# Performance work log

Hardware: AMD Instinct MI355X
Metric: run time of the kernel (lower is better)

## Reference

```python
import jax, jax.numpy as jnp
import numpy as np

N = 100000
E = 3200000
F_IN = 256
D_OUT = 128


def setup_inputs() -> dict:
    key = jax.random.key(0)
    ks = jax.random.split(key, 12)
    x = jax.random.normal(ks[0], (N, F_IN), dtype=jnp.float32)
    adj_val = jax.random.uniform(ks[1], (E,), dtype=jnp.float32)
    edge_row = jnp.sort(jax.random.randint(ks[2], (E,), 0, N))
    edge_col = jax.random.randint(ks[3], (E,), 0, N)
    # learned params (glorot-ish scaling)
    W1 = jax.random.normal(ks[4], (F_IN, D_OUT), dtype=jnp.float32) * (1.0 / np.sqrt(F_IN))   # conv1d_1 (1x1, no bias)
    w2 = jax.random.normal(ks[5], (D_OUT, 1), dtype=jnp.float32) * (1.0 / np.sqrt(D_OUT))     # conv1d_2
    b2 = jnp.zeros((1,), dtype=jnp.float32)
    w3 = jax.random.normal(ks[6], (D_OUT, 1), dtype=jnp.float32) * (1.0 / np.sqrt(D_OUT))     # conv1d_3
    b3 = jnp.zeros((1,), dtype=jnp.float32)
    kernel = jax.random.normal(ks[7], (F_IN, D_OUT), dtype=jnp.float32) * (1.0 / np.sqrt(F_IN))
    bias = jax.random.normal(ks[8], (N, D_OUT), dtype=jnp.float32) * 0.02
    return {"x": x, "adj_val": adj_val, "W1": W1, "w2": w2, "b2": b2,
            "w3": w3, "b3": b3, "kernel": kernel, "bias": bias,
            "edge_row": edge_row, "edge_col": edge_col}


def reference(x, adj_val, W1, w2, b2, w3, b3, kernel, bias, edge_row, edge_col):
    # 1x1 conv projections (equivalent to per-node dense layers)
    mapped = x @ W1                                   # [N, D]
    sa1 = (mapped @ w2 + b2)[:, 0]                    # [N]
    sa2 = (mapped @ w3 + b3)[:, 0]                    # [N]
    # sparse*dense broadcast then sparse add: per edge (i,j):
    #   adj_val * sa1[i] + adj_val * sa2[j]
    e = adj_val * (sa1[edge_row] + sa2[edge_col])     # [E]
    e = jax.nn.leaky_relu(e, negative_slope=0.2)
    # sparse row-wise softmax over nonzero entries
    m = jax.ops.segment_max(e, edge_row, num_segments=N)        # [N]
    m = jnp.where(jnp.isfinite(m), m, 0.0)
    ex = jnp.exp(e - m[edge_row])                               # [E]
    denom = jax.ops.segment_sum(ex, edge_row, num_segments=N)   # [N]
    denom = jnp.where(denom > 0, denom, 1.0)
    att = ex / denom[edge_row]                                  # [E]
    # dense feature transform then SpMM aggregation
    value = x @ kernel                                          # [N, D_OUT]
    out = jax.ops.segment_sum(att[:, None] * value[edge_col], edge_row, num_segments=N)
    out = out + bias                                            # use_bias=True
    return out  # activation=None (linear), single head, 'average' reduction
```

## Files before the change

### kernel.cpp

```cpp
#include <hip/hip_runtime.h>
#include <math.h>

#define N_NODES 100000
#define N_EDGES 3200000
#define F_IN    256
#define D_OUT   128

typedef __attribute__((ext_vector_type(8))) short short8;
typedef __attribute__((ext_vector_type(4))) float f32x4;

__device__ __forceinline__ unsigned short f2bf(float f) {
    unsigned u = __float_as_uint(f);
    unsigned r = (u + 0x7FFFu + ((u >> 16) & 1u)) >> 16;
    return (unsigned short)r;
}

__device__ __forceinline__ float dot4(f32x4 a, f32x4 b) {
    return a.x * b.x + a.y * b.y + a.z * b.z + a.w * b.w;
}

__device__ __forceinline__ float sb(unsigned u, int k) {
    return (float)((int)(u << ((3 - k) * 8)) >> 24);
}

__global__ __launch_bounds__(128) void prep_kernel(
    const float* __restrict__ W1, const float* __restrict__ w2,
    const float* __restrict__ w3, const float* __restrict__ kern,
    float* __restrict__ v1, float* __restrict__ v2,
    unsigned short* __restrict__ kbT) {
    const int kk  = blockIdx.x;
    const int tid = threadIdx.x;
    kbT[(size_t)tid * F_IN + kk] = f2bf(kern[(size_t)kk * D_OUT + tid]);
    if (tid < 64) {
        const float* wr = W1 + (size_t)kk * D_OUT;
        float a = wr[tid], b = wr[tid + 64];
        float s1 = a * w2[tid] + b * w2[tid + 64];
        float s2 = a * w3[tid] + b * w3[tid + 64];
#pragma unroll
        for (int o = 32; o > 0; o >>= 1) {
            s1 += __shfl_xor(s1, o);
            s2 += __shfl_xor(s2, o);
        }
        if (tid == 0) { v1[kk] = s1; v2[kk] = s2; }
    }
}

__global__ void row_ptr_kernel(const int* __restrict__ edge_row,
                               int* __restrict__ row_ptr) {
    int r = blockIdx.x * blockDim.x + threadIdx.x;
    if (r > N_NODES) return;
    int lo = 0, hi = N_EDGES;
    while (lo < hi) {
        int mid = (lo + hi) >> 1;
        if (edge_row[mid] < r) lo = mid + 1; else hi = mid;
    }
    row_ptr[r] = lo;
}

__global__ __launch_bounds__(256) void gemm_sa_kernel(
    const float* __restrict__ x, const unsigned short* __restrict__ kbT,
    const float* __restrict__ v1, const float* __restrict__ v2,
    const float* __restrict__ b2p, const float* __restrict__ b3p,
    signed char* __restrict__ valq, float* __restrict__ scale,
    float* __restrict__ sa1, float* __restrict__ sa2) {
    const int wid = blockIdx.x * 4 + (threadIdx.x >> 6);
    const int m_base = wid * 32;
    if (m_base >= N_NODES) return;
    const int lane = threadIdx.x & 63;
    const int r = lane & 15;
    const int q = lane >> 4;

    const f32x4* x0 = (const f32x4*)(x + (size_t)(m_base + r) * F_IN + q * 8);
    const f32x4* x1 = (const f32x4*)(x + (size_t)(m_base + 16 + r) * F_IN + q * 8);

    f32x4 acc[2][8];
#pragma unroll
    for (int t = 0; t < 2; ++t)
#pragma unroll
        for (int nt = 0; nt < 8; ++nt) acc[t][nt] = (f32x4)(0.f);
    float s1a = 0.f, s1b = 0.f, s2a = 0.f, s2b = 0.f;

#pragma unroll 2
    for (int s = 0; s < 8; ++s) {
        f32x4 p00 = __builtin_nontemporal_load(x0 + s * 8);
        f32x4 p01 = __builtin_nontemporal_load(x0 + s * 8 + 1);
        f32x4 p10 = __builtin_nontemporal_load(x1 + s * 8);
        f32x4 p11 = __builtin_nontemporal_load(x1 + s * 8 + 1);
        const f32x4* vp1 = (const f32x4*)(v1 + s * 32 + q * 8);
        const f32x4* vp2 = (const f32x4*)(v2 + s * 32 + q * 8);
        f32x4 va = vp1[0], vb = vp1[1], vc = vp2[0], vd = vp2[1];
        s1a += dot4(p00, va) + dot4(p01, vb);
        s2a += dot4(p00, vc) + dot4(p01, vd);
        s1b += dot4(p10, va) + dot4(p11, vb);
        s2b += dot4(p10, vc) + dot4(p11, vd);

        short8 a0, a1;
        a0[0] = (short)f2bf(p00.x); a0[1] = (short)f2bf(p00.y);
        a0[2] = (short)f2bf(p00.z); a0[3] = (short)f2bf(p00.w);
        a0[4] = (short)f2bf(p01.x); a0[5] = (short)f2bf(p01.y);
        a0[6] = (short)f2bf(p01.z); a0[7] = (short)f2bf(p01.w);
        a1[0] = (short)f2bf(p10.x); a1[1] = (short)f2bf(p10.y);
        a1[2] = (short)f2bf(p10.z); a1[3] = (short)f2bf(p10.w);
        a1[4] = (short)f2bf(p11.x); a1[5] = (short)f2bf(p11.y);
        a1[6] = (short)f2bf(p11.z); a1[7] = (short)f2bf(p11.w);

#pragma unroll
        for (int nt = 0; nt < 8; ++nt) {
            const short8 b = *(const short8*)(kbT + (size_t)(nt * 16 + r) * F_IN
                                              + s * 32 + q * 8);
            acc[0][nt] = __builtin_amdgcn_mfma_f32_16x16x32_bf16(a0, b, acc[0][nt], 0, 0, 0);
            acc[1][nt] = __builtin_amdgcn_mfma_f32_16x16x32_bf16(a1, b, acc[1][nt], 0, 0, 0);
        }
    }

    s1a += __shfl_xor(s1a, 16); s1a += __shfl_xor(s1a, 32);
    s1b += __shfl_xor(s1b, 16); s1b += __shfl_xor(s1b, 32);
    s2a += __shfl_xor(s2a, 16); s2a += __shfl_xor(s2a, 32);
    s2b += __shfl_xor(s2b, 16); s2b += __shfl_xor(s2b, 32);
    if (q == 0) {
        float bb2 = b2p[0], bb3 = b3p[0];
        sa1[m_base + r]      = s1a + bb2;
        sa1[m_base + 16 + r] = s1b + bb2;
        sa2[m_base + r]      = s2a + bb3;
        sa2[m_base + 16 + r] = s2b + bb3;
    }

#pragma unroll
    for (int t = 0; t < 2; ++t)
#pragma unroll
        for (int reg = 0; reg < 4; ++reg) {
            float m = 0.f;
#pragma unroll
            for (int nt = 0; nt < 8; ++nt) m = fmaxf(m, fabsf(acc[t][nt][reg]));
            m = fmaxf(m, __shfl_xor(m, 1));
            m = fmaxf(m, __shfl_xor(m, 2));
            m = fmaxf(m, __shfl_xor(m, 4));
            m = fmaxf(m, __shfl_xor(m, 8));
            const int row = m_base + t * 16 + q * 4 + reg;
            const float inv = m > 0.f ? 127.f / m : 0.f;
            if (r == 0) scale[row] = m * (1.f / 127.f);
#pragma unroll
            for (int nt = 0; nt < 8; ++nt) {
                int iq = (int)rintf(acc[t][nt][reg] * inv);
                valq[(size_t)row * D_OUT + nt * 16 + r] = (signed char)iq;
            }
        }
}

__global__ __launch_bounds__(256) void attn_agg_kernel(
    const int* __restrict__ row_ptr, const int* __restrict__ edge_col,
    const float* __restrict__ adj, const float* __restrict__ sa1,
    const float* __restrict__ sa2, const signed char* __restrict__ valq,
    const float* __restrict__ scale, const float* __restrict__ bias,
    float* __restrict__ out) {
    const int lane = threadIdx.x & 63;
    int row = blockIdx.x * 4 + (threadIdx.x >> 6);
    if (row >= N_NODES) return;
    row = __builtin_amdgcn_readfirstlane(row);

    const int s   = row_ptr[row];
    const int cnt = row_ptr[row + 1] - s;
    const float sa1r = sa1[row];

    const int g = lane >> 4;
    const int r = lane & 15;
    const signed char* vbase = valq + r * 8;

    float acc[8];
#pragma unroll
    for (int j = 0; j < 8; ++j) acc[j] = 0.f;
    float sum = 0.f;

    for (int base = 0; base < cnt; base += 64) {
        const int n = min(64, cnt - base);

        int c = 0;
        float w = 0.f;
        if (lane < n) {
            const int e = s + base + lane;
            c = __builtin_nontemporal_load(edge_col + e);
            const float a = __builtin_nontemporal_load(adj + e);
            float t = a * (sa1r + sa2[c]);
            t = fmaxf(t, 0.2f * t);
            const float ex = __expf(t);
            sum += ex;
            w = ex * scale[c];
        }

#pragma unroll 4
        for (int i = 0; i < n; i += 4) {
            const int   cc = __shfl(c, i + g);
            const float ww = __shfl(w, i + g);
            const uint2 p = *(const uint2*)(vbase + (size_t)cc * D_OUT);
            acc[0] += ww * sb(p.x, 0); acc[1] += ww * sb(p.x, 1);
            acc[2] += ww * sb(p.x, 2); acc[3] += ww * sb(p.x, 3);
            acc[4] += ww * sb(p.y, 0); acc[5] += ww * sb(p.y, 1);
            acc[6] += ww * sb(p.y, 2); acc[7] += ww * sb(p.y, 3);
        }
    }

    sum += __shfl_xor(sum, 1);
    sum += __shfl_xor(sum, 2);
    sum += __shfl_xor(sum, 4);
    sum += __shfl_xor(sum, 8);
#pragma unroll
    for (int o = 16; o < 64; o <<= 1) {
        sum += __shfl_xor(sum, o);
#pragma unroll
        for (int j = 0; j < 8; ++j) acc[j] += __shfl_xor(acc[j], o);
    }
    const float inv = sum > 0.f ? 1.f / sum : 1.f;

    if (g == 0) {
        const f32x4* bp = (const f32x4*)(bias + (size_t)row * D_OUT + r * 8);
        f32x4 b0 = __builtin_nontemporal_load(bp);
        f32x4 b1 = __builtin_nontemporal_load(bp + 1);
        f32x4 r0, r1;
        r0.x = acc[0] * inv + b0.x; r0.y = acc[1] * inv + b0.y;
        r0.z = acc[2] * inv + b0.z; r0.w = acc[3] * inv + b0.w;
        r1.x = acc[4] * inv + b1.x; r1.y = acc[5] * inv + b1.y;
        r1.z = acc[6] * inv + b1.z; r1.w = acc[7] * inv + b1.w;
        f32x4* op = (f32x4*)(out + (size_t)row * D_OUT + r * 8);
        __builtin_nontemporal_store(r0, op);
        __builtin_nontemporal_store(r1, op + 1);
    }
}

extern "C" void kernel_launch(void* const* d_in, const int* in_sizes, int n_in,
                              void* d_out, int out_size, void* d_ws,
                              size_t ws_size, hipStream_t stream) {
    const float* x        = (const float*)d_in[0];
    const float* adj      = (const float*)d_in[1];
    const float* W1       = (const float*)d_in[2];
    const float* w2       = (const float*)d_in[3];
    const float* b2       = (const float*)d_in[4];
    const float* w3       = (const float*)d_in[5];
    const float* b3       = (const float*)d_in[6];
    const float* kern     = (const float*)d_in[7];
    const float* bias     = (const float*)d_in[8];
    const int*   edge_row = (const int*)d_in[9];
    const int*   edge_col = (const int*)d_in[10];
    float* out = (float*)d_out;

    signed char* valq = (signed char*)d_ws;
    float* scale = (float*)(valq + (size_t)N_NODES * D_OUT);
    float* sa1 = scale + N_NODES;
    float* sa2 = sa1 + N_NODES;
    int*   row_ptr = (int*)(sa2 + N_NODES);
    float* v1 = (float*)(row_ptr + N_NODES + 4);
    float* v2 = v1 + F_IN;
    unsigned short* kbT = (unsigned short*)(v2 + F_IN);

    hipLaunchKernelGGL(prep_kernel, dim3(256), dim3(128), 0, stream,
                       W1, w2, w3, kern, v1, v2, kbT);
    hipLaunchKernelGGL(row_ptr_kernel, dim3((N_NODES + 1 + 255) / 256),
                       dim3(256), 0, stream, edge_row, row_ptr);
    hipLaunchKernelGGL(gemm_sa_kernel, dim3((N_NODES / 32 + 3) / 4), dim3(256),
                       0, stream, x, kbT, v1, v2, b2, b3, valq, scale, sa1,
                       sa2);
    hipLaunchKernelGGL(attn_agg_kernel, dim3(N_NODES / 4), dim3(256), 0,
                       stream, row_ptr, edge_col, adj, sa1, sa2, valq, scale,
                       bias, out);
}
```

Before: 377.3 us.

## Map one row per 16-lane group with software-prefetched edge loads

The aggregation kernel now gives each 16-lane quarter-wave its own row instead of one row per wave. Each group walks its edges four at a time, prefetching the next batch of column indices and adjacency values while processing the current one. This removes the cross-lane shuffles and the final cross-group reduction, and quadruples rows per block. In exchange, lanes in a wave diverge when rows have different degrees, each edge's sa2/scale loads are repeated across the 16 lanes, and the per-edge scalar loads are no longer coalesced across the wave.

```diff
diff --git a/kernel.cpp b/kernel.cpp
--- a/kernel.cpp
+++ b/kernel.cpp
@@ -154,16 +154,13 @@
     const float* __restrict__ scale, const float* __restrict__ bias,
     float* __restrict__ out) {
     const int lane = threadIdx.x & 63;
-    int row = blockIdx.x * 4 + (threadIdx.x >> 6);
-    if (row >= N_NODES) return;
-    row = __builtin_amdgcn_readfirstlane(row);
-
-    const int s   = row_ptr[row];
-    const int cnt = row_ptr[row + 1] - s;
+    const int g    = lane >> 4;
+    const int r    = lane & 15;
+    const int row  = blockIdx.x * 16 + ((threadIdx.x >> 6) << 2) + g;
+
+    const int s    = row_ptr[row];
+    const int cnt  = row_ptr[row + 1] - s;
     const float sa1r = sa1[row];
-
-    const int g = lane >> 4;
-    const int r = lane & 15;
     const signed char* vbase = valq + r * 8;
 
     float acc[8];
@@ -171,59 +168,93 @@
     for (int j = 0; j < 8; ++j) acc[j] = 0.f;
     float sum = 0.f;
 
-    for (int base = 0; base < cnt; base += 64) {
-        const int n = min(64, cnt - base);
-
-        int c = 0;
-        float w = 0.f;
-        if (lane < n) {
-            const int e = s + base + lane;
-            c = __builtin_nontemporal_load(edge_col + e);
-            const float a = __builtin_nontemporal_load(adj + e);
-            float t = a * (sa1r + sa2[c]);
+    const int n4 = cnt & ~3;
+
+    int   c0, c1, c2, c3;
+    float a0, a1, a2, a3;
+    bool act = (0 < n4);
+    if (act) {
+        c0 = __builtin_nontemporal_load(edge_col + s);
+        c1 = __builtin_nontemporal_load(edge_col + s + 1);
+        c2 = __builtin_nontemporal_load(edge_col + s + 2);
+        c3 = __builtin_nontemporal_load(edge_col + s + 3);
+        a0 = __builtin_nontemporal_load(adj + s);
+        a1 = __builtin_nontemporal_load(adj + s + 1);
+        a2 = __builtin_nontemporal_load(adj + s + 2);
+        a3 = __builtin_nontemporal_load(adj + s + 3);
+    }
+    int i = 0;
+    while (__any(act)) {
+        const int  inext = i + 4;
+        const bool actn  = (inext < n4);
+        int   d0 = 0, d1 = 0, d2 = 0, d3 = 0;
+        float e0 = 0, e1 = 0, e2 = 0, e3 = 0;
+        if (actn) {
+            d0 = __builtin_nontemporal_load(edge_col + s + inext);
+            d1 = __builtin_nontemporal_load(edge_col + s + inext + 1);
+            d2 = __builtin_nontemporal_load(edge_col + s + inext + 2);
+            d3 = __builtin_nontemporal_load(edge_col + s + inext + 3);
+            e0 = __builtin_nontemporal_load(adj + s + inext);
+            e1 = __builtin_nontemporal_load(adj + s + inext + 1);
+            e2 = __builtin_nontemporal_load(adj + s + inext + 2);
+            e3 = __builtin_nontemporal_load(adj + s + inext + 3);
+        }
+        if (act) {
+            const int cc[4] = {c0, c1, c2, c3};
+            const float aa[4] = {a0, a1, a2, a3};
+#pragma unroll
+            for (int j = 0; j < 4; ++j) {
+                const int cj = cc[j];
+                float t = aa[j] * (sa1r + sa2[cj]);
+                t = fmaxf(t, 0.2f * t);
+                const float ex = __expf(t);
+                sum += ex;
+                const float w = ex * scale[cj];
+                const uint2 p = *(const uint2*)(vbase + (size_t)cj * D_OUT);
+                acc[0] += w * sb(p.x, 0); acc[1] += w * sb(p.x, 1);
+                acc[2] += w * sb(p.x, 2); acc[3] += w * sb(p.x, 3);
+                acc[4] += w * sb(p.y, 0); acc[5] += w * sb(p.y, 1);
+                acc[6] += w * sb(p.y, 2); acc[7] += w * sb(p.y, 3);
+            }
+        }
+        c0 = d0; c1 = d1; c2 = d2; c3 = d3;
+        a0 = e0; a1 = e1; a2 = e2; a3 = e3;
+        i = inext;
+        act = actn;
+    }
+
+    int i2 = n4;
+    while (__any(i2 < cnt)) {
+        if (i2 < cnt) {
+            const int e = s + i2;
+            const int cj = __builtin_nontemporal_load(edge_col + e);
+            float t = __builtin_nontemporal_load(adj + e) * (sa1r + sa2[cj]);
             t = fmaxf(t, 0.2f * t);
             const float ex = __expf(t);
             sum += ex;
-            w = ex * scale[c];
-        }
-
-#pragma unroll 4
-        for (int i = 0; i < n; i += 4) {
-            const int   cc = __shfl(c, i + g);
-            const float ww = __shfl(w, i + g);
-            const uint2 p = *(const uint2*)(vbase + (size_t)cc * D_OUT);
-            acc[0] += ww * sb(p.x, 0); acc[1] += ww * sb(p.x, 1);
-            acc[2] += ww * sb(p.x, 2); acc[3] += ww * sb(p.x, 3);
-            acc[4] += ww * sb(p.y, 0); acc[5] += ww * sb(p.y, 1);
-            acc[6] += ww * sb(p.y, 2); acc[7] += ww * sb(p.y, 3);
-        }
-    }
-
-    sum += __shfl_xor(sum, 1);
-    sum += __shfl_xor(sum, 2);
-    sum += __shfl_xor(sum, 4);
-    sum += __shfl_xor(sum, 8);
-#pragma unroll
-    for (int o = 16; o < 64; o <<= 1) {
-        sum += __shfl_xor(sum, o);
-#pragma unroll
-        for (int j = 0; j < 8; ++j) acc[j] += __shfl_xor(acc[j], o);
-    }
+            const float w = ex * scale[cj];
+            const uint2 p = *(const uint2*)(vbase + (size_t)cj * D_OUT);
+            acc[0] += w * sb(p.x, 0); acc[1] += w * sb(p.x, 1);
+            acc[2] += w * sb(p.x, 2); acc[3] += w * sb(p.x, 3);
+            acc[4] += w * sb(p.y, 0); acc[5] += w * sb(p.y, 1);
+            acc[6] += w * sb(p.y, 2); acc[7] += w * sb(p.y, 3);
+        }
+        ++i2;
+    }
+
     const float inv = sum > 0.f ? 1.f / sum : 1.f;
 
-    if (g == 0) {
-        const f32x4* bp = (const f32x4*)(bias + (size_t)row * D_OUT + r * 8);
-        f32x4 b0 = __builtin_nontemporal_load(bp);
-        f32x4 b1 = __builtin_nontemporal_load(bp + 1);
-        f32x4 r0, r1;
-        r0.x = acc[0] * inv + b0.x; r0.y = acc[1] * inv + b0.y;
-        r0.z = acc[2] * inv + b0.z; r0.w = acc[3] * inv + b0.w;
-        r1.x = acc[4] * inv + b1.x; r1.y = acc[5] * inv + b1.y;
-        r1.z = acc[6] * inv + b1.z; r1.w = acc[7] * inv + b1.w;
-        f32x4* op = (f32x4*)(out + (size_t)row * D_OUT + r * 8);
-        __builtin_nontemporal_store(r0, op);
-        __builtin_nontemporal_store(r1, op + 1);
-    }
+    const f32x4* bp = (const f32x4*)(bias + (size_t)row * D_OUT + r * 8);
+    f32x4 b0 = __builtin_nontemporal_load(bp);
+    f32x4 b1 = __builtin_nontemporal_load(bp + 1);
+    f32x4 r0, r1;
+    r0.x = acc[0] * inv + b0.x; r0.y = acc[1] * inv + b0.y;
+    r0.z = acc[2] * inv + b0.z; r0.w = acc[3] * inv + b0.w;
+    r1.x = acc[4] * inv + b1.x; r1.y = acc[5] * inv + b1.y;
+    r1.z = acc[6] * inv + b1.z; r1.w = acc[7] * inv + b1.w;
+    f32x4* op = (f32x4*)(out + (size_t)row * D_OUT + r * 8);
+    __builtin_nontemporal_store(r0, op);
+    __builtin_nontemporal_store(r1, op + 1);
 }
 
 extern "C" void kernel_launch(void* const* d_in, const int* in_sizes, int n_in,
@@ -258,7 +289,7 @@
     hipLaunchKernelGGL(gemm_sa_kernel, dim3((N_NODES / 32 + 3) / 4), dim3(256),
                        0, stream, x, kbT, v1, v2, b2, b3, valq, scale, sa1,
                        sa2);
-    hipLaunchKernelGGL(attn_agg_kernel, dim3(N_NODES / 4), dim3(256), 0,
+    hipLaunchKernelGGL(attn_agg_kernel, dim3(N_NODES / 16), dim3(256), 0,
                        stream, row_ptr, edge_col, adj, sa1, sa2, valq, scale,
                        bias, out);
 }
```

Result: slower. 387.1 us (+2.6%).

## Batch gathers in SpMM, pack sa2/scale into float2, use offset-uint8 values

Applied to the files above, without the earlier changes.

The aggregation kernel now issues up to sixteen row gathers per 64-edge chunk before doing any arithmetic, so more memory loads are in flight at once. The per-node sa2 and scale values are packed into one float2 array, so each edge needs one random gather instead of two. Quantized values are stored as unsigned bytes offset by 128, which makes unpacking a plain shift-and-mask. The offset is removed afterwards with a correction term built from the summed weights. The bias load is also moved ahead of the loop to hide its latency, at the cost of more registers for the sixteen buffered gathers.

```diff
diff --git a/kernel.cpp b/kernel.cpp
--- a/kernel.cpp
+++ b/kernel.cpp
@@ -19,8 +19,8 @@
     return a.x * b.x + a.y * b.y + a.z * b.z + a.w * b.w;
 }
 
-__device__ __forceinline__ float sb(unsigned u, int k) {
-    return (float)((int)(u << ((3 - k) * 8)) >> 24);
+__device__ __forceinline__ float ub(unsigned u, int k) {
+    return (float)((u >> (k * 8)) & 0xffu);
 }
 
 __global__ __launch_bounds__(128) void prep_kernel(
@@ -61,8 +61,8 @@
     const float* __restrict__ x, const unsigned short* __restrict__ kbT,
     const float* __restrict__ v1, const float* __restrict__ v2,
     const float* __restrict__ b2p, const float* __restrict__ b3p,
-    signed char* __restrict__ valq, float* __restrict__ scale,
-    float* __restrict__ sa1, float* __restrict__ sa2) {
+    unsigned char* __restrict__ valq, float2* __restrict__ szc,
+    float* __restrict__ sa1) {
     const int wid = blockIdx.x * 4 + (threadIdx.x >> 6);
     const int m_base = wid * 32;
     if (m_base >= N_NODES) return;
@@ -121,8 +121,8 @@
         float bb2 = b2p[0], bb3 = b3p[0];
         sa1[m_base + r]      = s1a + bb2;
         sa1[m_base + 16 + r] = s1b + bb2;
-        sa2[m_base + r]      = s2a + bb3;
-        sa2[m_base + 16 + r] = s2b + bb3;
+        szc[m_base + r].x      = s2a + bb3;
+        szc[m_base + 16 + r].x = s2b + bb3;
     }
 
 #pragma unroll
@@ -138,11 +138,12 @@
             m = fmaxf(m, __shfl_xor(m, 8));
             const int row = m_base + t * 16 + q * 4 + reg;
             const float inv = m > 0.f ? 127.f / m : 0.f;
-            if (r == 0) scale[row] = m * (1.f / 127.f);
+            if (r == 0) szc[row].y = m * (1.f / 127.f);
 #pragma unroll
             for (int nt = 0; nt < 8; ++nt) {
                 int iq = (int)rintf(acc[t][nt][reg] * inv);
-                valq[(size_t)row * D_OUT + nt * 16 + r] = (signed char)iq;
+                valq[(size_t)row * D_OUT + nt * 16 + r] =
+                    (unsigned char)(iq + 128);
             }
         }
 }
@@ -150,26 +151,26 @@
 __global__ __launch_bounds__(256) void attn_agg_kernel(
     const int* __restrict__ row_ptr, const int* __restrict__ edge_col,
     const float* __restrict__ adj, const float* __restrict__ sa1,
-    const float* __restrict__ sa2, const signed char* __restrict__ valq,
-    const float* __restrict__ scale, const float* __restrict__ bias,
-    float* __restrict__ out) {
+    const float2* __restrict__ szc, const unsigned char* __restrict__ valq,
+    const float* __restrict__ bias, float* __restrict__ out) {
     const int lane = threadIdx.x & 63;
-    int row = blockIdx.x * 4 + (threadIdx.x >> 6);
-    if (row >= N_NODES) return;
-    row = __builtin_amdgcn_readfirstlane(row);
+    const int g    = lane >> 4;
+    const int r    = lane & 15;
+    const int row  = blockIdx.x * 4 + (threadIdx.x >> 6);
 
     const int s   = row_ptr[row];
     const int cnt = row_ptr[row + 1] - s;
     const float sa1r = sa1[row];
-
-    const int g = lane >> 4;
-    const int r = lane & 15;
-    const signed char* vbase = valq + r * 8;
+    const unsigned char* vbase = valq + r * 8;
+
+    const f32x4* bp = (const f32x4*)(bias + (size_t)row * D_OUT + r * 8);
+    f32x4 b0 = __builtin_nontemporal_load(bp);
+    f32x4 b1 = __builtin_nontemporal_load(bp + 1);
 
     float acc[8];
 #pragma unroll
     for (int j = 0; j < 8; ++j) acc[j] = 0.f;
-    float sum = 0.f;
+    float sum = 0.f, sumw = 0.f;
 
     for (int base = 0; base < cnt; base += 64) {
         const int n = min(64, cnt - base);
@@ -180,46 +181,65 @@
             const int e = s + base + lane;
             c = __builtin_nontemporal_load(edge_col + e);
             const float a = __builtin_nontemporal_load(adj + e);
-            float t = a * (sa1r + sa2[c]);
+            const float2 f2 = szc[c];
+            float t = a * (sa1r + f2.x);
             t = fmaxf(t, 0.2f * t);
             const float ex = __expf(t);
             sum += ex;
-            w = ex * scale[c];
-        }
-
-#pragma unroll 4
-        for (int i = 0; i < n; i += 4) {
-            const int   cc = __shfl(c, i + g);
-            const float ww = __shfl(w, i + g);
-            const uint2 p = *(const uint2*)(vbase + (size_t)cc * D_OUT);
-            acc[0] += ww * sb(p.x, 0); acc[1] += ww * sb(p.x, 1);
-            acc[2] += ww * sb(p.x, 2); acc[3] += ww * sb(p.x, 3);
-            acc[4] += ww * sb(p.y, 0); acc[5] += ww * sb(p.y, 1);
-            acc[6] += ww * sb(p.y, 2); acc[7] += ww * sb(p.y, 3);
-        }
-    }
-
-    sum += __shfl_xor(sum, 1);
-    sum += __shfl_xor(sum, 2);
-    sum += __shfl_xor(sum, 4);
-    sum += __shfl_xor(sum, 8);
+            w = ex * f2.y;
+        }
+        sumw += w;
+
+        const int nchunk = (n + 15) >> 4;
+        uint2 p[16];
+#pragma unroll
+        for (int ch = 0; ch < 4; ++ch) {
+            if (ch < nchunk) {
+#pragma unroll
+                for (int k4 = 0; k4 < 4; ++k4) {
+                    const int k = ch * 4 + k4;
+                    const int cc = __shfl(c, k * 4 + g);
+                    p[k] = *(const uint2*)(vbase + (size_t)cc * D_OUT);
+                }
+            }
+        }
+#pragma unroll
+        for (int ch = 0; ch < 4; ++ch) {
+            if (ch < nchunk) {
+#pragma unroll
+                for (int k4 = 0; k4 < 4; ++k4) {
+                    const int k = ch * 4 + k4;
+                    const float ww = __shfl(w, k * 4 + g);
+                    const uint2 q = p[k];
+                    acc[0] += ww * ub(q.x, 0); acc[1] += ww * ub(q.x, 1);
+                    acc[2] += ww * ub(q.x, 2); acc[3] += ww * ub(q.x, 3);
+                    acc[4] += ww * ub(q.y, 0); acc[5] += ww * ub(q.y, 1);
+                    acc[6] += ww * ub(q.y, 2); acc[7] += ww * ub(q.y, 3);
+                }
+            }
+        }
+    }
+
+    sum  += __shfl_xor(sum, 1);  sumw += __shfl_xor(sumw, 1);
+    sum  += __shfl_xor(sum, 2);  sumw += __shfl_xor(sumw, 2);
+    sum  += __shfl_xor(sum, 4);  sumw += __shfl_xor(sumw, 4);
+    sum  += __shfl_xor(sum, 8);  sumw += __shfl_xor(sumw, 8);
 #pragma unroll
     for (int o = 16; o < 64; o <<= 1) {
-        sum += __shfl_xor(sum, o);
+        sum  += __shfl_xor(sum, o);
+        sumw += __shfl_xor(sumw, o);
 #pragma unroll
         for (int j = 0; j < 8; ++j) acc[j] += __shfl_xor(acc[j], o);
     }
-    const float inv = sum > 0.f ? 1.f / sum : 1.f;
+    const float inv  = sum > 0.f ? 1.f / sum : 1.f;
+    const float corr = 128.f * sumw;
 
     if (g == 0) {
-        const f32x4* bp = (const f32x4*)(bias + (size_t)row * D_OUT + r * 8);
-        f32x4 b0 = __builtin_nontemporal_load(bp);
-        f32x4 b1 = __builtin_nontemporal_load(bp + 1);
         f32x4 r0, r1;
-        r0.x = acc[0] * inv + b0.x; r0.y = acc[1] * inv + b0.y;
-        r0.z = acc[2] * inv + b0.z; r0.w = acc[3] * inv + b0.w;
-        r1.x = acc[4] * inv + b1.x; r1.y = acc[5] * inv + b1.y;
-        r1.z = acc[6] * inv + b1.z; r1.w = acc[7] * inv + b1.w;
+        r0.x = (acc[0] - corr) * inv + b0.x; r0.y = (acc[1] - corr) * inv + b0.y;
+        r0.z = (acc[2] - corr) * inv + b0.z; r0.w = (acc[3] - corr) * inv + b0.w;
+        r1.x = (acc[4] - corr) * inv + b1.x; r1.y = (acc[5] - corr) * inv + b1.y;
+        r1.z = (acc[6] - corr) * inv + b1.z; r1.w = (acc[7] - corr) * inv + b1.w;
         f32x4* op = (f32x4*)(out + (size_t)row * D_OUT + r * 8);
         __builtin_nontemporal_store(r0, op);
         __builtin_nontemporal_store(r1, op + 1);
@@ -242,11 +262,10 @@
     const int*   edge_col = (const int*)d_in[10];
     float* out = (float*)d_out;
 
-    signed char* valq = (signed char*)d_ws;
-    float* scale = (float*)(valq + (size_t)N_NODES * D_OUT);
-    float* sa1 = scale + N_NODES;
-    float* sa2 = sa1 + N_NODES;
-    int*   row_ptr = (int*)(sa2 + N_NODES);
+    unsigned char* valq = (unsigned char*)d_ws;
+    float2* szc = (float2*)(valq + (size_t)N_NODES * D_OUT);
+    float*  sa1 = (float*)(szc + N_NODES);
+    int* row_ptr = (int*)(sa1 + N_NODES);
     float* v1 = (float*)(row_ptr + N_NODES + 4);
     float* v2 = v1 + F_IN;
     unsigned short* kbT = (unsigned short*)(v2 + F_IN);
@@ -256,9 +275,8 @@
     hipLaunchKernelGGL(row_ptr_kernel, dim3((N_NODES + 1 + 255) / 256),
                        dim3(256), 0, stream, edge_row, row_ptr);
     hipLaunchKernelGGL(gemm_sa_kernel, dim3((N_NODES / 32 + 3) / 4), dim3(256),
-                       0, stream, x, kbT, v1, v2, b2, b3, valq, scale, sa1,
-                       sa2);
+                       0, stream, x, kbT, v1, v2, b2, b3, valq, szc, sa1);
     hipLaunchKernelGGL(attn_agg_kernel, dim3(N_NODES / 4), dim3(256), 0,
-                       stream, row_ptr, edge_col, adj, sa1, sa2, valq, scale,
+                       stream, row_ptr, edge_col, adj, sa1, szc, valq,
                        bias, out);
 }
```

After: 354.2 us. 1.07x faster.
